# Performance work log

Hardware: AMD Instinct MI355X
Metric: run time of the kernel (lower is better)

Reference implementation:

```python
import jax, jax.numpy as jnp
import numpy as np

B, D_IN, EMB = 8192, 4000, 96
H0, H1 = 2048, 1024
NB, NC, OPT = 8, 8, 32
NE = NB * NC  # 64 experts (total contests)


def setup_inputs() -> dict:
    key = jax.random.key(0)
    ks = jax.random.split(key, 10)
    scale = lambda fan_in: jnp.sqrt(2.0 / fan_in)  # kaiming_normal-ish
    return {
        "inputs": jax.random.normal(ks[0], (B, D_IN), dtype=jnp.float32),
        "emb_table": jax.random.normal(ks[1], (NE, EMB), dtype=jnp.float32) * scale(EMB),
        "W0": jax.random.normal(ks[2], (D_IN + EMB, H0), dtype=jnp.float32) * scale(D_IN + EMB),
        "b0": jnp.zeros((H0,), dtype=jnp.float32),
        "W1": jax.random.normal(ks[3], (H0, H1), dtype=jnp.float32) * scale(H0),
        "b1": jnp.zeros((H1,), dtype=jnp.float32),
        "We": jax.random.normal(ks[4], (NE, H1, OPT), dtype=jnp.float32) * scale(H1),
        "be": jnp.zeros((NE, OPT), dtype=jnp.float32),
        "ballot_number": jax.random.randint(ks[5], (B,), 0, NB, dtype=jnp.int32),
        "contest_number": jax.random.randint(ks[6], (B,), 0, NC, dtype=jnp.int32),
        "batches": B,
    }


def reference(inputs, emb_table, W0, b0, W1, b1, We, be,
              ballot_number, contest_number, batches):
    # flat expert index per sample: index_of[ballot][contest] with equal-size ballots
    expert = ballot_number * NC + contest_number                  # [B]
    x = inputs.reshape(batches, -1)                               # [B, D_IN]
    emb = emb_table[expert]                                       # [B, EMB] (gather)
    h = jnp.concatenate([emb, x], axis=1)                         # [B, D_IN+EMB]
    h = jax.nn.relu(h @ W0 + b0)                                  # fc0 (dropout = id at eval)
    h = jax.nn.relu(h @ W1 + b1)                                  # fc1
    # per-sample routed linear: gather expert weights, batched matvec
    out = jnp.einsum("bd,bdo->bo", h, We[expert]) + be[expert]    # [B, OPT]
    return jax.nn.sigmoid(out)
```

## Files before the change

### kernel.cpp

```cpp
#include <hip/hip_runtime.h>
#include <math.h>

typedef __attribute__((ext_vector_type(8))) short short8;
typedef __attribute__((ext_vector_type(4))) float f32x4;

#define B_SZ 8192
#define D_INN 4000
#define EMBD 96
#define H0D 2048
#define H1D 1024
#define KDIM 4096

__device__ __forceinline__ unsigned short f2bf(float f) {
  union { float f; unsigned u; } v; v.f = f;
  unsigned r = v.u + 0x7FFFu + ((v.u >> 16) & 1u);
  return (unsigned short)(r >> 16);
}
__device__ __forceinline__ float bf2f(unsigned short h) {
  union { unsigned u; float f; } v; v.u = ((unsigned)h) << 16;
  return v.f;
}
__device__ __forceinline__ void gld_lds16(const void* g, void* l) {
  __builtin_amdgcn_global_load_lds(
      (const __attribute__((address_space(1))) unsigned int*)g,
      (__attribute__((address_space(3))) unsigned int*)l, 16, 0, 0);
}

__global__ __launch_bounds__(256) void transpose_cvt(
    const float* __restrict__ in, unsigned short* __restrict__ out, int R, int C) {
  __shared__ float tile[32][33];
  int c0 = blockIdx.x * 32, r0 = blockIdx.y * 32;
  int tc = threadIdx.x & 31, tr = threadIdx.x >> 5;
#pragma unroll
  for (int i = 0; i < 4; ++i) {
    int r = tr + i * 8;
    tile[r][tc] = in[(size_t)(r0 + r) * C + (c0 + tc)];
  }
  __syncthreads();
#pragma unroll
  for (int i = 0; i < 4; ++i) {
    int rr = tr + i * 8;
    out[(size_t)(c0 + rr) * R + (r0 + tc)] = f2bf(tile[tc][rr]);
  }
}

__global__ __launch_bounds__(256) void build_A(
    const float* __restrict__ inputs, const float* __restrict__ emb,
    const int* __restrict__ ballot, const int* __restrict__ contest,
    unsigned short* __restrict__ A) {
  int gid = blockIdx.x * 256 + threadIdx.x;
  int b = gid >> 9, c = gid & 511;
  const float* src;
  if (c < EMBD / 8) {
    int e = ballot[b] * 8 + contest[b];
    src = emb + (size_t)e * EMBD + c * 8;
  } else {
    src = inputs + (size_t)b * D_INN + (c - EMBD / 8) * 8;
  }
  float4 v0 = *(const float4*)src;
  float4 v1 = *(const float4*)(src + 4);
  unsigned short r[8];
  r[0] = f2bf(v0.x); r[1] = f2bf(v0.y); r[2] = f2bf(v0.z); r[3] = f2bf(v0.w);
  r[4] = f2bf(v1.x); r[5] = f2bf(v1.y); r[6] = f2bf(v1.z); r[7] = f2bf(v1.w);
  *reinterpret_cast<short8*>(A + (size_t)b * KDIM + c * 8) =
      *reinterpret_cast<const short8*>(r);
}

template <int MREP>
__global__ __launch_bounds__(512, 2) void gemm_nt_pipe(
    const unsigned short* __restrict__ A, const unsigned short* __restrict__ Bt,
    const float* __restrict__ bias, unsigned short* __restrict__ C,
    int K, int N, int NBN) {
  constexpr int BM  = MREP * 32;
  constexpr int AI  = MREP / 4;
  constexpr int ASH = MREP * 1024;
  constexpr int NLD = AI + 2;
  __shared__ unsigned short lds[3 * ASH + 3 * 8192];

  const int tid = threadIdx.x;
  const int w = tid >> 6, l = tid & 63;
  const int lr = l & 15, kg = l >> 4;
  const int wm = w >> 2, wn = w & 3;

  int swz = (blockIdx.x & 7) * ((int)gridDim.x >> 3) + ((int)blockIdx.x >> 3);
  const int bm = swz / NBN, bn = swz - bm * NBN;
  const int NT = K >> 5;

  const int rg = l >> 2;
  const int sl = ((l & 3) ^ ((l >> 3) & 3)) * 8;
  const unsigned short* ga[AI];
#pragma unroll
  for (int i = 0; i < AI; ++i)
    ga[i] = A + (size_t)(bm * BM + (i * 8 + w) * 16 + rg) * K + sl;
  const unsigned short* gb[2];
#pragma unroll
  for (int j = 0; j < 2; ++j)
    gb[j] = Bt + (size_t)(bn * 256 + (j * 8 + w) * 16 + rg) * K + sl;

  const int xo = (kg ^ ((lr >> 1) & 3)) << 4;
  const int aoff = (wm * (MREP * 16) + lr) * 64 + xo;
  const int boff = (wn * 64 + lr) * 64 + xo;

  f32x4 acc[MREP][4] = {};

  auto stage = [&](int t, int rbuf) {
    unsigned short* la = lds + rbuf * ASH + w * 512;
    unsigned short* lb = lds + 3 * ASH + rbuf * 8192 + w * 512;
    const int ko = t * 32;
#pragma unroll
    for (int i = 0; i < AI; ++i) gld_lds16(ga[i] + ko, la + i * 4096);
    gld_lds16(gb[0] + ko, lb);
    gld_lds16(gb[1] + ko, lb + 4096);
  };

  stage(0, 0);
  stage(1, 1);
  if constexpr (NLD == 4) asm volatile("s_waitcnt vmcnt(4)" ::: "memory");
  else                    asm volatile("s_waitcnt vmcnt(3)" ::: "memory");
  __builtin_amdgcn_s_barrier();
  __builtin_amdgcn_sched_barrier(0);

  int rb = 0;
  for (int t = 0; t < NT; ++t) {
    int rb2 = rb + 2; if (rb2 >= 3) rb2 -= 3;
    if (t + 2 < NT) stage(t + 2, rb2);

    const char* pa = (const char*)lds + rb * (ASH * 2) + aoff;
    const char* pb = (const char*)lds + 6 * ASH + rb * 16384 + boff;
    short8 a[MREP], b[4];
#pragma unroll
    for (int mi = 0; mi < MREP; ++mi) a[mi] = *(const short8*)(pa + mi * 1024);
#pragma unroll
    for (int ni = 0; ni < 4; ++ni)   b[ni] = *(const short8*)(pb + ni * 1024);

    __builtin_amdgcn_s_setprio(1);
#pragma unroll
    for (int mi = 0; mi < MREP; ++mi)
#pragma unroll
      for (int ni = 0; ni < 4; ++ni)
        acc[mi][ni] = __builtin_amdgcn_mfma_f32_16x16x32_bf16(
            a[mi], b[ni], acc[mi][ni], 0, 0, 0);
    __builtin_amdgcn_s_setprio(0);

    __builtin_amdgcn_sched_barrier(0);
    asm volatile("s_waitcnt lgkmcnt(0)" ::: "memory");
    if (t + 2 < NT) {
      if constexpr (NLD == 4) asm volatile("s_waitcnt vmcnt(4)" ::: "memory");
      else                    asm volatile("s_waitcnt vmcnt(3)" ::: "memory");
      __builtin_amdgcn_s_barrier();
    } else if (t + 1 < NT) {
      asm volatile("s_waitcnt vmcnt(0)" ::: "memory");
      __builtin_amdgcn_s_barrier();
    }
    __builtin_amdgcn_sched_barrier(0);

    rb = rb + 1; if (rb >= 3) rb = 0;
  }

#pragma unroll
  for (int mi = 0; mi < MREP; ++mi) {
    const int row0 = bm * BM + wm * (MREP * 16) + mi * 16 + kg * 4;
#pragma unroll
    for (int ni = 0; ni < 4; ++ni) {
      const int col = bn * 256 + wn * 64 + ni * 16 + lr;
      const float bv = bias[col];
#pragma unroll
      for (int j = 0; j < 4; ++j) {
        float v = acc[mi][ni][j] + bv;
        v = v > 0.f ? v : 0.f;
        C[(size_t)(row0 + j) * N + col] = f2bf(v);
      }
    }
  }
}

__global__ __launch_bounds__(256) void expert_head(
    const unsigned short* __restrict__ h1, const float* __restrict__ We,
    const float* __restrict__ be, const int* __restrict__ ballot,
    const int* __restrict__ contest, float* __restrict__ out) {
  int b = blockIdx.x * 4 + (threadIdx.x >> 6);
  int lane = threadIdx.x & 63;
  int o = lane & 31, half = lane >> 5;
  int e = ballot[b] * 8 + contest[b];
  const unsigned short* hrow = h1 + (size_t)b * H1D + half * 512;
  const float* wb = We + ((size_t)e * H1D + half * 512) * 32 + o;
  float acc = 0.f;
  for (int d0 = 0; d0 < 512; d0 += 8) {
    short8 hv = *reinterpret_cast<const short8*>(&hrow[d0]);
#pragma unroll
    for (int j = 0; j < 8; ++j)
      acc = fmaf(bf2f((unsigned short)hv[j]), wb[(size_t)(d0 + j) * 32], acc);
  }
  acc += __shfl_xor(acc, 32, 64);
  if (half == 0) {
    float x = acc + be[e * 32 + o];
    out[(size_t)b * 32 + o] = 1.f / (1.f + expf(-x));
  }
}

extern "C" void kernel_launch(void* const* d_in, const int* in_sizes, int n_in,
                              void* d_out, int out_size, void* d_ws, size_t ws_size,
                              hipStream_t stream) {
  const float* inputs = (const float*)d_in[0];
  const float* emb    = (const float*)d_in[1];
  const float* W0     = (const float*)d_in[2];
  const float* b0     = (const float*)d_in[3];
  const float* W1     = (const float*)d_in[4];
  const float* b1     = (const float*)d_in[5];
  const float* We     = (const float*)d_in[6];
  const float* be     = (const float*)d_in[7];
  const int* ballot   = (const int*)d_in[8];
  const int* contest  = (const int*)d_in[9];
  float* out = (float*)d_out;

  char* ws = (char*)d_ws;
  unsigned short* A   = (unsigned short*)(ws);
  unsigned short* W0t = (unsigned short*)(ws + 67108864);
  unsigned short* h0  = (unsigned short*)(ws + 83886080);
  unsigned short* W1t = (unsigned short*)(ws + 117440512);
  unsigned short* h1  = (unsigned short*)(ws + 121634816);

  dim3 blk(256);
  transpose_cvt<<<dim3(H0D / 32, KDIM / 32, 1), blk, 0, stream>>>(W0, W0t, KDIM, H0D);
  transpose_cvt<<<dim3(H1D / 32, H0D / 32, 1), blk, 0, stream>>>(W1, W1t, H0D, H1D);
  build_A<<<dim3(B_SZ * 512 / 256), blk, 0, stream>>>(inputs, emb, ballot, contest, A);
  gemm_nt_pipe<8><<<dim3((B_SZ / 256) * (H0D / 256)), dim3(512), 0, stream>>>(
      A, W0t, b0, h0, KDIM, H0D, H0D / 256);
  gemm_nt_pipe<4><<<dim3((B_SZ / 128) * (H1D / 256)), dim3(512), 0, stream>>>(
      h0, W1t, b1, h1, H0D, H1D, H1D / 256);
  expert_head<<<dim3(B_SZ / 4), blk, 0, stream>>>(h1, We, be, ballot, contest, out);
}
```

Baseline: 265.2 us.

## Retile GEMMs to 256-thread blocks and bucket expert head by expert

The GEMM kernel is generalized over block and warp tile shapes and launched with 256 threads. fc0 moves from 256x256 to 128x256 tiles and fc1 from 128x256 to 128x128. LDS fragment reads are now issued before the next stage's global loads, to overlap better. The expert head is replaced by a kernel that buckets samples per expert into LDS, so each expert's weights are streamed once per block instead of once per sample, at the cost of a serial scan with atomics.

```diff
diff --git a/kernel.cpp b/kernel.cpp
--- a/kernel.cpp
+++ b/kernel.cpp
@@ -66,21 +66,22 @@
       *reinterpret_cast<const short8*>(r);
 }
 
-template <int MREP>
-__global__ __launch_bounds__(512, 2) void gemm_nt_pipe(
+template <int BM, int BN, int WM, int WN>
+__global__ __launch_bounds__(256, 2) void gemm_nt_pipe(
     const unsigned short* __restrict__ A, const unsigned short* __restrict__ Bt,
     const float* __restrict__ bias, unsigned short* __restrict__ C,
     int K, int N, int NBN) {
-  constexpr int BM  = MREP * 32;
-  constexpr int AI  = MREP / 4;
-  constexpr int ASH = MREP * 1024;
-  constexpr int NLD = AI + 2;
-  __shared__ unsigned short lds[3 * ASH + 3 * 8192];
+  constexpr int MREP = BM / (WM * 16);
+  constexpr int NREP = BN / (WN * 16);
+  constexpr int AR = BM / 64, BR = BN / 64;
+  constexpr int NLD = AR + BR;
+  constexpr int AB = BM * 64, BB = BN * 64;
+  __shared__ char lds[3 * (AB + BB)];
 
   const int tid = threadIdx.x;
   const int w = tid >> 6, l = tid & 63;
   const int lr = l & 15, kg = l >> 4;
-  const int wm = w >> 2, wn = w & 3;
+  const int wm = w / WN, wn = w % WN;
 
   int swz = (blockIdx.x & 7) * ((int)gridDim.x >> 3) + ((int)blockIdx.x >> 3);
   const int bm = swz / NBN, bn = swz - bm * NBN;
@@ -88,72 +89,68 @@
 
   const int rg = l >> 2;
   const int sl = ((l & 3) ^ ((l >> 3) & 3)) * 8;
-  const unsigned short* ga[AI];
-#pragma unroll
-  for (int i = 0; i < AI; ++i)
-    ga[i] = A + (size_t)(bm * BM + (i * 8 + w) * 16 + rg) * K + sl;
-  const unsigned short* gb[2];
-#pragma unroll
-  for (int j = 0; j < 2; ++j)
-    gb[j] = Bt + (size_t)(bn * 256 + (j * 8 + w) * 16 + rg) * K + sl;
+  const unsigned short* gaB = A + (size_t)(bm * BM + w * 16 + rg) * K + sl;
+  const unsigned short* gbB = Bt + (size_t)(bn * BN + w * 16 + rg) * K + sl;
 
   const int xo = (kg ^ ((lr >> 1) & 3)) << 4;
   const int aoff = (wm * (MREP * 16) + lr) * 64 + xo;
-  const int boff = (wn * 64 + lr) * 64 + xo;
-
-  f32x4 acc[MREP][4] = {};
-
-  auto stage = [&](int t, int rbuf) {
-    unsigned short* la = lds + rbuf * ASH + w * 512;
-    unsigned short* lb = lds + 3 * ASH + rbuf * 8192 + w * 512;
-    const int ko = t * 32;
-#pragma unroll
-    for (int i = 0; i < AI; ++i) gld_lds16(ga[i] + ko, la + i * 4096);
-    gld_lds16(gb[0] + ko, lb);
-    gld_lds16(gb[1] + ko, lb + 4096);
+  const int boff = (wn * (NREP * 16) + lr) * 64 + xo;
+
+  f32x4 acc[MREP][NREP] = {};
+
+  auto stage = [&](int t, int slot) {
+    char* la = lds + slot * AB + w * 1024;
+    char* lb = lds + 3 * AB + slot * BB + w * 1024;
+    const size_t ko = (size_t)t * 32;
+#pragma unroll
+    for (int i = 0; i < AR; ++i)
+      gld_lds16(gaB + (size_t)i * 64 * K + ko, la + i * 4096);
+#pragma unroll
+    for (int j = 0; j < BR; ++j)
+      gld_lds16(gbB + (size_t)j * 64 * K + ko, lb + j * 4096);
   };
+
+#define WAIT_STEADY() do { \
+    if constexpr (NLD == 6) asm volatile("s_waitcnt vmcnt(6)" ::: "memory"); \
+    else                    asm volatile("s_waitcnt vmcnt(4)" ::: "memory"); \
+  } while (0)
 
   stage(0, 0);
   stage(1, 1);
-  if constexpr (NLD == 4) asm volatile("s_waitcnt vmcnt(4)" ::: "memory");
-  else                    asm volatile("s_waitcnt vmcnt(3)" ::: "memory");
+  WAIT_STEADY();
   __builtin_amdgcn_s_barrier();
   __builtin_amdgcn_sched_barrier(0);
 
   int rb = 0;
   for (int t = 0; t < NT; ++t) {
     int rb2 = rb + 2; if (rb2 >= 3) rb2 -= 3;
+    const char* pa = lds + rb * AB + aoff;
+    const char* pb = lds + 3 * AB + rb * BB + boff;
+    short8 af[MREP], bfr[NREP];
+#pragma unroll
+    for (int mi = 0; mi < MREP; ++mi) af[mi] = *(const short8*)(pa + mi * 1024);
+#pragma unroll
+    for (int ni = 0; ni < NREP; ++ni) bfr[ni] = *(const short8*)(pb + ni * 1024);
     if (t + 2 < NT) stage(t + 2, rb2);
-
-    const char* pa = (const char*)lds + rb * (ASH * 2) + aoff;
-    const char* pb = (const char*)lds + 6 * ASH + rb * 16384 + boff;
-    short8 a[MREP], b[4];
-#pragma unroll
-    for (int mi = 0; mi < MREP; ++mi) a[mi] = *(const short8*)(pa + mi * 1024);
-#pragma unroll
-    for (int ni = 0; ni < 4; ++ni)   b[ni] = *(const short8*)(pb + ni * 1024);
-
+    asm volatile("s_waitcnt lgkmcnt(0)" ::: "memory");
+    __builtin_amdgcn_sched_barrier(0);
     __builtin_amdgcn_s_setprio(1);
 #pragma unroll
     for (int mi = 0; mi < MREP; ++mi)
 #pragma unroll
-      for (int ni = 0; ni < 4; ++ni)
+      for (int ni = 0; ni < NREP; ++ni)
         acc[mi][ni] = __builtin_amdgcn_mfma_f32_16x16x32_bf16(
-            a[mi], b[ni], acc[mi][ni], 0, 0, 0);
+            af[mi], bfr[ni], acc[mi][ni], 0, 0, 0);
     __builtin_amdgcn_s_setprio(0);
-
     __builtin_amdgcn_sched_barrier(0);
-    asm volatile("s_waitcnt lgkmcnt(0)" ::: "memory");
     if (t + 2 < NT) {
-      if constexpr (NLD == 4) asm volatile("s_waitcnt vmcnt(4)" ::: "memory");
-      else                    asm volatile("s_waitcnt vmcnt(3)" ::: "memory");
+      WAIT_STEADY();
       __builtin_amdgcn_s_barrier();
     } else if (t + 1 < NT) {
       asm volatile("s_waitcnt vmcnt(0)" ::: "memory");
       __builtin_amdgcn_s_barrier();
     }
     __builtin_amdgcn_sched_barrier(0);
-
     rb = rb + 1; if (rb >= 3) rb = 0;
   }
 
@@ -161,8 +158,8 @@
   for (int mi = 0; mi < MREP; ++mi) {
     const int row0 = bm * BM + wm * (MREP * 16) + mi * 16 + kg * 4;
 #pragma unroll
-    for (int ni = 0; ni < 4; ++ni) {
-      const int col = bn * 256 + wn * 64 + ni * 16 + lr;
+    for (int ni = 0; ni < NREP; ++ni) {
+      const int col = bn * BN + wn * (NREP * 16) + ni * 16 + lr;
       const float bv = bias[col];
 #pragma unroll
       for (int j = 0; j < 4; ++j) {
@@ -172,29 +169,57 @@
       }
     }
   }
-}
-
-__global__ __launch_bounds__(256) void expert_head(
+#undef WAIT_STEADY
+}
+
+__global__ __launch_bounds__(256) void expert_head_bucketed(
     const unsigned short* __restrict__ h1, const float* __restrict__ We,
     const float* __restrict__ be, const int* __restrict__ ballot,
     const int* __restrict__ contest, float* __restrict__ out) {
-  int b = blockIdx.x * 4 + (threadIdx.x >> 6);
-  int lane = threadIdx.x & 63;
-  int o = lane & 31, half = lane >> 5;
-  int e = ballot[b] * 8 + contest[b];
-  const unsigned short* hrow = h1 + (size_t)b * H1D + half * 512;
-  const float* wb = We + ((size_t)e * H1D + half * 512) * 32 + o;
-  float acc = 0.f;
-  for (int d0 = 0; d0 < 512; d0 += 8) {
-    short8 hv = *reinterpret_cast<const short8*>(&hrow[d0]);
-#pragma unroll
-    for (int j = 0; j < 8; ++j)
-      acc = fmaf(bf2f((unsigned short)hv[j]), wb[(size_t)(d0 + j) * 32], acc);
-  }
-  acc += __shfl_xor(acc, 32, 64);
-  if (half == 0) {
-    float x = acc + be[e * 32 + o];
-    out[(size_t)b * 32 + o] = 1.f / (1.f + expf(-x));
+  const int e = blockIdx.x >> 2, q = blockIdx.x & 3;
+  __shared__ unsigned short sidx[2048];
+  __shared__ int scnt;
+  __shared__ unsigned short sh1[32][1032];
+  if (threadIdx.x == 0) scnt = 0;
+  __syncthreads();
+  const int base = q * 2048;
+  for (int i = threadIdx.x; i < 2048; i += 256) {
+    int s = base + i;
+    if (ballot[s] * 8 + contest[s] == e)
+      sidx[atomicAdd(&scnt, 1)] = (unsigned short)s;
+  }
+  __syncthreads();
+  const int cnt = scnt;
+  const int so = threadIdx.x >> 3;
+  const int oq = threadIdx.x & 7;
+  const float4* We4 = (const float4*)(We + (size_t)e * H1D * 32);
+  for (int c0 = 0; c0 < cnt; c0 += 32) {
+    const int ns = min(32, cnt - c0);
+    __syncthreads();
+    for (int t = threadIdx.x; t < ns * 128; t += 256) {
+      int r = t >> 7, cc = (t & 127) * 8;
+      *(short8*)&sh1[r][cc] =
+          *(const short8*)&h1[(size_t)sidx[c0 + r] * H1D + cc];
+    }
+    __syncthreads();
+    if (so < ns) {
+      const int s = sidx[c0 + so];
+      float ax = 0.f, ay = 0.f, az = 0.f, aw = 0.f;
+#pragma unroll 8
+      for (int d = 0; d < H1D; ++d) {
+        float h = bf2f(sh1[so][d]);
+        float4 wv = We4[d * 8 + oq];
+        ax = fmaf(h, wv.x, ax); ay = fmaf(h, wv.y, ay);
+        az = fmaf(h, wv.z, az); aw = fmaf(h, wv.w, aw);
+      }
+      float4 bb = *(const float4*)&be[e * 32 + oq * 4];
+      float4 r;
+      r.x = 1.f / (1.f + expf(-(ax + bb.x)));
+      r.y = 1.f / (1.f + expf(-(ay + bb.y)));
+      r.z = 1.f / (1.f + expf(-(az + bb.z)));
+      r.w = 1.f / (1.f + expf(-(aw + bb.w)));
+      *(float4*)&out[(size_t)s * 32 + oq * 4] = r;
+    }
   }
 }
 
@@ -224,9 +249,9 @@
   transpose_cvt<<<dim3(H0D / 32, KDIM / 32, 1), blk, 0, stream>>>(W0, W0t, KDIM, H0D);
   transpose_cvt<<<dim3(H1D / 32, H0D / 32, 1), blk, 0, stream>>>(W1, W1t, H0D, H1D);
   build_A<<<dim3(B_SZ * 512 / 256), blk, 0, stream>>>(inputs, emb, ballot, contest, A);
-  gemm_nt_pipe<8><<<dim3((B_SZ / 256) * (H0D / 256)), dim3(512), 0, stream>>>(
+  gemm_nt_pipe<128, 256, 1, 4><<<dim3(512), blk, 0, stream>>>(
       A, W0t, b0, h0, KDIM, H0D, H0D / 256);
-  gemm_nt_pipe<4><<<dim3((B_SZ / 128) * (H1D / 256)), dim3(512), 0, stream>>>(
-      h0, W1t, b1, h1, H0D, H1D, H1D / 256);
-  expert_head<<<dim3(B_SZ / 4), blk, 0, stream>>>(h1, We, be, ballot, contest, out);
-}
+  gemm_nt_pipe<128, 128, 2, 2><<<dim3(512), blk, 0, stream>>>(
+      h0, W1t, b1, h1, H0D, H1D, H1D / 128);
+  expert_head_bucketed<<<dim3(256), blk, 0, stream>>>(h1, We, be, ballot, contest, out);
+}
```

Result: slower. 307.2 us (+15.8%).
